# Kernel optimization log

Measured on AMD Instinct MI355X. Metric: run time of the kernel, lower is better.

The kernel has to match this reference:

```python
import jax, jax.numpy as jnp
import numpy as np

B, D = 200000, 128
K = 1024


def setup_inputs() -> dict:
    key = jax.random.key(0)
    k1, k2 = jax.random.split(key)
    x_BD = jax.random.normal(k1, (B, D), dtype=jnp.float32)
    codebook = jax.random.uniform(k2, (K, D), dtype=jnp.float32)
    return {"x_BD": x_BD, "codebook": codebook}


def reference(x_BD, codebook):
    x_sq_B1 = jnp.sum(x_BD * x_BD, axis=-1, keepdims=True)
    c_sq_K = jnp.sum(codebook * codebook, axis=-1)
    dists_BK = x_sq_B1 - 2.0 * jnp.einsum("bd,kd->bk", x_BD, codebook) + c_sq_K
    codes_B = jnp.argmin(dists_BK, axis=-1)  # [B] int
    quant_x_BD = codebook[codes_B]           # gather, [B, D]
    return quant_x_BD, codes_B
```

## Files before the change

### kernel.cpp

```cpp
#include <hip/hip_runtime.h>


typedef float v2f __attribute__((ext_vector_type(2)));

#define DDIM 128
#define KCODES 1024
#define BM 64
#define BN 256
#define DCH 16
#define NTILES (KCODES / BN)
#define NCHUNK (DDIM / DCH)

__global__ void csq_kernel(const float* __restrict__ cb, float* __restrict__ csq) {
    int k = blockIdx.x * blockDim.x + threadIdx.x;
    if (k >= KCODES) return;
    const float* __restrict__ c = cb + (long)k * DDIM;
    float s0 = 0.f, s1 = 0.f, s2 = 0.f, s3 = 0.f;
#pragma unroll
    for (int d = 0; d < DDIM; d += 4) {
        s0 = fmaf(c[d + 0], c[d + 0], s0);
        s1 = fmaf(c[d + 1], c[d + 1], s1);
        s2 = fmaf(c[d + 2], c[d + 2], s2);
        s3 = fmaf(c[d + 3], c[d + 3], s3);
    }
    csq[k] = (s0 + s1) + (s2 + s3);
}

#define PK_LO(a, xx, cc) \
    asm("v_pk_fma_f32 %0, %1, %2, %0 op_sel:[0,0,0] op_sel_hi:[0,1,1]" \
        : "+v"(a) : "v"(xx), "v"(cc))
#define PK_HI(a, xx, cc) \
    asm("v_pk_fma_f32 %0, %1, %2, %0 op_sel:[1,0,0] op_sel_hi:[1,1,1]" \
        : "+v"(a) : "v"(xx), "v"(cc))

__launch_bounds__(256, 3)
__global__ void vq_gemm_kernel(const float* __restrict__ x, const float* __restrict__ cb,
                               const float* __restrict__ csq, float* __restrict__ quant,
                               float* __restrict__ codes) {
    __shared__ float xs[DDIM * BM];
    __shared__ float cs[DCH * BN];
    __shared__ int win[BM];

    const int tid = threadIdx.x;
    const long r0 = (long)blockIdx.x * BM;

    {
        const int r = tid >> 2;
        const int qb = (tid & 3) * 8;
        const float* __restrict__ xrow = x + (r0 + r) * DDIM;
#pragma unroll
        for (int j = 0; j < 8; ++j) {
            const int q = qb + j;
            const float4 v = *(const float4*)(xrow + q * 4);
            xs[(q * 4 + 0) * BM + r] = v.x;
            xs[(q * 4 + 1) * BM + r] = v.y;
            xs[(q * 4 + 2) * BM + r] = v.z;
            xs[(q * 4 + 3) * BM + r] = v.w;
        }
    }
    __syncthreads();

    const int tr = tid >> 5;
    const int tc = tid & 31;

    float s[4][8];
#pragma unroll
    for (int a = 0; a < 4; ++a)
#pragma unroll
        for (int b = 0; b < 8; ++b) s[a][b] = 0.f;
#pragma unroll
    for (int d = 0; d < DDIM; d += 4) {
#pragma unroll
        for (int dd = 0; dd < 4; ++dd) {
            const float4 a0 = *(const float4*)&xs[(d + dd) * BM + tr * 8];
            const float4 a1 = *(const float4*)&xs[(d + dd) * BM + tr * 8 + 4];
            s[dd][0] = fmaf(a0.x, a0.x, s[dd][0]);
            s[dd][1] = fmaf(a0.y, a0.y, s[dd][1]);
            s[dd][2] = fmaf(a0.z, a0.z, s[dd][2]);
            s[dd][3] = fmaf(a0.w, a0.w, s[dd][3]);
            s[dd][4] = fmaf(a1.x, a1.x, s[dd][4]);
            s[dd][5] = fmaf(a1.y, a1.y, s[dd][5]);
            s[dd][6] = fmaf(a1.z, a1.z, s[dd][6]);
            s[dd][7] = fmaf(a1.w, a1.w, s[dd][7]);
        }
    }
    float xsq[8];
#pragma unroll
    for (int i = 0; i < 8; ++i) xsq[i] = (s[0][i] + s[1][i]) + (s[2][i] + s[3][i]);

    float best[8];
    int bidx[8];
#pragma unroll
    for (int i = 0; i < 8; ++i) { best[i] = 3.4e38f; bidx[i] = 0; }

#pragma unroll 1
    for (int ct = 0; ct < NTILES; ++ct) {
        v2f acc[8][4];
#pragma unroll
        for (int i = 0; i < 8; ++i)
#pragma unroll
            for (int jj = 0; jj < 4; ++jj) acc[i][jj] = (v2f){0.f, 0.f};

#pragma unroll 1
        for (int dc = 0; dc < NCHUNK; ++dc) {
            __syncthreads();
            {
                const float* __restrict__ crow =
                    cb + (long)(ct * BN + tid) * DDIM + dc * DCH;
#pragma unroll
                for (int j = 0; j < 4; ++j) {
                    const float4 v = *(const float4*)(crow + j * 4);
                    cs[(j * 4 + 0) * BN + tid] = v.x;
                    cs[(j * 4 + 1) * BN + tid] = v.y;
                    cs[(j * 4 + 2) * BN + tid] = v.z;
                    cs[(j * 4 + 3) * BN + tid] = v.w;
                }
            }
            __syncthreads();
#pragma unroll
            for (int d = 0; d < DCH; ++d) {
                const float4 xa0 = *(const float4*)&xs[(dc * DCH + d) * BM + tr * 8];
                const float4 xa1 = *(const float4*)&xs[(dc * DCH + d) * BM + tr * 8 + 4];
                const float4 ca0 = *(const float4*)&cs[d * BN + tc * 4];
                const float4 ca1 = *(const float4*)&cs[d * BN + 128 + tc * 4];
                v2f xp[4], cp[4];
                xp[0] = (v2f){xa0.x, xa0.y}; xp[1] = (v2f){xa0.z, xa0.w};
                xp[2] = (v2f){xa1.x, xa1.y}; xp[3] = (v2f){xa1.z, xa1.w};
                cp[0] = (v2f){ca0.x, ca0.y}; cp[1] = (v2f){ca0.z, ca0.w};
                cp[2] = (v2f){ca1.x, ca1.y}; cp[3] = (v2f){ca1.z, ca1.w};
#pragma unroll
                for (int jj = 0; jj < 4; ++jj) {
                    PK_LO(acc[0][jj], xp[0], cp[jj]);
                    PK_HI(acc[1][jj], xp[0], cp[jj]);
                    PK_LO(acc[2][jj], xp[1], cp[jj]);
                    PK_HI(acc[3][jj], xp[1], cp[jj]);
                    PK_LO(acc[4][jj], xp[2], cp[jj]);
                    PK_HI(acc[5][jj], xp[2], cp[jj]);
                    PK_LO(acc[6][jj], xp[3], cp[jj]);
                    PK_HI(acc[7][jj], xp[3], cp[jj]);
                }
            }
        }

        float csq_r[8];
#pragma unroll
        for (int j = 0; j < 4; ++j) {
            csq_r[j]     = csq[ct * BN + tc * 4 + j];
            csq_r[4 + j] = csq[ct * BN + 128 + tc * 4 + j];
        }
#pragma unroll
        for (int i = 0; i < 8; ++i) {
#pragma unroll
            for (int jj = 0; jj < 4; ++jj) {
#pragma unroll
                for (int h = 0; h < 2; ++h) {
                    const int jl = jj * 2 + h;
                    const int cj = ct * BN + ((jl < 4) ? (tc * 4 + jl) : (128 + tc * 4 + jl - 4));
                    const float dist = fmaf(-2.0f, acc[i][jj][h], xsq[i]) + csq_r[jl];
                    if (dist < best[i]) { best[i] = dist; bidx[i] = cj; }
                }
            }
        }
    }

#pragma unroll
    for (int i = 0; i < 8; ++i) {
#pragma unroll
        for (int off = 16; off >= 1; off >>= 1) {
            const float ov = __shfl_xor(best[i], off);
            const int ovi = __shfl_xor(bidx[i], off);
            if (ov < best[i] || (ov == best[i] && ovi < bidx[i])) {
                best[i] = ov; bidx[i] = ovi;
            }
        }
    }
    if (tc == 0) {
#pragma unroll
        for (int i = 0; i < 8; ++i) {
            const int r = tr * 8 + i;
            codes[r0 + r] = (float)bidx[i];
            win[r] = bidx[i];
        }
    }
    __syncthreads();

    {
        const int r = tid >> 2;
        const int qb = (tid & 3) * 8;
        const float* __restrict__ crow = cb + (long)win[r] * DDIM;
        float* __restrict__ qrow = quant + (r0 + r) * DDIM;
#pragma unroll
        for (int j = 0; j < 8; ++j) {
            const int q = qb + j;
            *(float4*)(qrow + q * 4) = *(const float4*)(crow + q * 4);
        }
    }
}

extern "C" void kernel_launch(void* const* d_in, const int* in_sizes, int n_in,
                              void* d_out, int out_size, void* d_ws, size_t ws_size,
                              hipStream_t stream) {
    const float* x  = (const float*)d_in[0];
    const float* cb = (const float*)d_in[1];
    const int B = in_sizes[0] / DDIM;

    float* quant = (float*)d_out;
    float* codes = (float*)d_out + (size_t)B * DDIM;
    float* csq   = (float*)d_ws;

    csq_kernel<<<(KCODES + 255) / 256, 256, 0, stream>>>(cb, csq);

    const int blocks = B / BM;
    vq_gemm_kernel<<<blocks, 256, 0, stream>>>(x, cb, csq, quant, codes);
}
```

Baseline: 791.2 us.

## Broadcast x rows via scalar loads, double-buffer codebook tiles in LDS

Each wavefront now owns 16 rows. The x values are fetched with s_load_dwordx2 into SGPRs and used as the scalar operand of v_pk_fma_f32, so the x tile is no longer staged in LDS. Codebook chunks are double-buffered in LDS with a register prefetch of the next chunk, which cuts the barriers per chunk from two to one. The row norms ||x||^2 are computed directly from global memory and broadcast with shuffles. The trade-offs are serialized scalar-load latency, since every sub-step waits on lgkmcnt(0), and more accumulator and register pressure.

```diff
diff --git a/kernel.cpp b/kernel.cpp
--- a/kernel.cpp
+++ b/kernel.cpp
@@ -2,6 +2,7 @@
 
 
 typedef float v2f __attribute__((ext_vector_type(2)));
+typedef int   v2i __attribute__((ext_vector_type(2)));
 
 #define DDIM 128
 #define KCODES 1024
@@ -26,161 +27,184 @@
     csq[k] = (s0 + s1) + (s2 + s3);
 }
 
-#define PK_LO(a, xx, cc) \
+#define PKL(a, xx, cc) \
     asm("v_pk_fma_f32 %0, %1, %2, %0 op_sel:[0,0,0] op_sel_hi:[0,1,1]" \
-        : "+v"(a) : "v"(xx), "v"(cc))
-#define PK_HI(a, xx, cc) \
+        : "+v"(a) : "s"(xx), "v"(cc))
+#define PKH(a, xx, cc) \
     asm("v_pk_fma_f32 %0, %1, %2, %0 op_sel:[1,0,0] op_sel_hi:[1,1,1]" \
-        : "+v"(a) : "v"(xx), "v"(cc))
+        : "+v"(a) : "s"(xx), "v"(cc))
+
+#define FOR16(M) M(0) M(1) M(2) M(3) M(4) M(5) M(6) M(7) \
+                 M(8) M(9) M(10) M(11) M(12) M(13) M(14) M(15)
 
 __launch_bounds__(256, 3)
 __global__ void vq_gemm_kernel(const float* __restrict__ x, const float* __restrict__ cb,
                                const float* __restrict__ csq, float* __restrict__ quant,
                                float* __restrict__ codes) {
-    __shared__ float xs[DDIM * BM];
-    __shared__ float cs[DCH * BN];
+    __shared__ float cs[2][DCH * BN];
     __shared__ int win[BM];
 
     const int tid = threadIdx.x;
     const long r0 = (long)blockIdx.x * BM;
+    const int lane = tid & 63;
+    const int wv = __builtin_amdgcn_readfirstlane(tid >> 6);
+    const int wr0 = wv * 16;
+
+    float xsq_mine = 0.f;
+    if (lane < 16) {
+        const float* __restrict__ xr = x + (r0 + wr0 + lane) * DDIM;
+        float s0 = 0.f, s1 = 0.f, s2 = 0.f, s3 = 0.f;
+#pragma unroll
+        for (int q = 0; q < 32; ++q) {
+            const float4 v = *(const float4*)(xr + q * 4);
+            s0 = fmaf(v.x, v.x, s0);
+            s1 = fmaf(v.y, v.y, s1);
+            s2 = fmaf(v.z, v.z, s2);
+            s3 = fmaf(v.w, v.w, s3);
+        }
+        xsq_mine = (s0 + s1) + (s2 + s3);
+    }
+    float xsqall[16];
+#pragma unroll
+    for (int r = 0; r < 16; ++r) xsqall[r] = __shfl(xsq_mine, r);
 
     {
-        const int r = tid >> 2;
-        const int qb = (tid & 3) * 8;
-        const float* __restrict__ xrow = x + (r0 + r) * DDIM;
-#pragma unroll
-        for (int j = 0; j < 8; ++j) {
-            const int q = qb + j;
-            const float4 v = *(const float4*)(xrow + q * 4);
-            xs[(q * 4 + 0) * BM + r] = v.x;
-            xs[(q * 4 + 1) * BM + r] = v.y;
-            xs[(q * 4 + 2) * BM + r] = v.z;
-            xs[(q * 4 + 3) * BM + r] = v.w;
+        const float* __restrict__ crow = cb + (long)tid * DDIM;
+#pragma unroll
+        for (int j = 0; j < 4; ++j) {
+            const float4 v = *(const float4*)(crow + j * 4);
+            cs[0][(j * 4 + 0) * BN + tid] = v.x;
+            cs[0][(j * 4 + 1) * BN + tid] = v.y;
+            cs[0][(j * 4 + 2) * BN + tid] = v.z;
+            cs[0][(j * 4 + 3) * BN + tid] = v.w;
         }
     }
     __syncthreads();
 
-    const int tr = tid >> 5;
-    const int tc = tid & 31;
-
-    float s[4][8];
-#pragma unroll
-    for (int a = 0; a < 4; ++a)
-#pragma unroll
-        for (int b = 0; b < 8; ++b) s[a][b] = 0.f;
-#pragma unroll
-    for (int d = 0; d < DDIM; d += 4) {
-#pragma unroll
-        for (int dd = 0; dd < 4; ++dd) {
-            const float4 a0 = *(const float4*)&xs[(d + dd) * BM + tr * 8];
-            const float4 a1 = *(const float4*)&xs[(d + dd) * BM + tr * 8 + 4];
-            s[dd][0] = fmaf(a0.x, a0.x, s[dd][0]);
-            s[dd][1] = fmaf(a0.y, a0.y, s[dd][1]);
-            s[dd][2] = fmaf(a0.z, a0.z, s[dd][2]);
-            s[dd][3] = fmaf(a0.w, a0.w, s[dd][3]);
-            s[dd][4] = fmaf(a1.x, a1.x, s[dd][4]);
-            s[dd][5] = fmaf(a1.y, a1.y, s[dd][5]);
-            s[dd][6] = fmaf(a1.z, a1.z, s[dd][6]);
-            s[dd][7] = fmaf(a1.w, a1.w, s[dd][7]);
-        }
-    }
-    float xsq[8];
-#pragma unroll
-    for (int i = 0; i < 8; ++i) xsq[i] = (s[0][i] + s[1][i]) + (s[2][i] + s[3][i]);
-
-    float best[8];
-    int bidx[8];
-#pragma unroll
-    for (int i = 0; i < 8; ++i) { best[i] = 3.4e38f; bidx[i] = 0; }
+    float best[16];
+    int bidx[16];
+#pragma unroll
+    for (int r = 0; r < 16; ++r) { best[r] = 3.4e38f; bidx[r] = 0; }
+
+    v2f acc[16][2];
 
 #pragma unroll 1
-    for (int ct = 0; ct < NTILES; ++ct) {
-        v2f acc[8][4];
-#pragma unroll
-        for (int i = 0; i < 8; ++i)
-#pragma unroll
-            for (int jj = 0; jj < 4; ++jj) acc[i][jj] = (v2f){0.f, 0.f};
-
+    for (int t = 0; t < NTILES * NCHUNK; ++t) {
+        const int ct = t >> 3;
+        const int dc = t & 7;
+        if (dc == 0) {
+#define ZA(R) acc[R][0] = (v2f){0.f, 0.f}; acc[R][1] = (v2f){0.f, 0.f};
+            FOR16(ZA)
+#undef ZA
+        }
+
+        float4 pf0, pf1, pf2, pf3;
+        if (t < NTILES * NCHUNK - 1) {
+            const int nt = t + 1;
+            const float* __restrict__ crow =
+                cb + (long)(((nt >> 3) * BN) + tid) * DDIM + (nt & 7) * DCH;
+            pf0 = *(const float4*)(crow + 0);
+            pf1 = *(const float4*)(crow + 4);
+            pf2 = *(const float4*)(crow + 8);
+            pf3 = *(const float4*)(crow + 12);
+        }
+
+        const float* csp = cs[t & 1];
 #pragma unroll 1
-        for (int dc = 0; dc < NCHUNK; ++dc) {
-            __syncthreads();
-            {
-                const float* __restrict__ crow =
-                    cb + (long)(ct * BN + tid) * DDIM + dc * DCH;
-#pragma unroll
-                for (int j = 0; j < 4; ++j) {
-                    const float4 v = *(const float4*)(crow + j * 4);
-                    cs[(j * 4 + 0) * BN + tid] = v.x;
-                    cs[(j * 4 + 1) * BN + tid] = v.y;
-                    cs[(j * 4 + 2) * BN + tid] = v.z;
-                    cs[(j * 4 + 3) * BN + tid] = v.w;
-                }
-            }
-            __syncthreads();
-#pragma unroll
-            for (int d = 0; d < DCH; ++d) {
-                const float4 xa0 = *(const float4*)&xs[(dc * DCH + d) * BM + tr * 8];
-                const float4 xa1 = *(const float4*)&xs[(dc * DCH + d) * BM + tr * 8 + 4];
-                const float4 ca0 = *(const float4*)&cs[d * BN + tc * 4];
-                const float4 ca1 = *(const float4*)&cs[d * BN + 128 + tc * 4];
-                v2f xp[4], cp[4];
-                xp[0] = (v2f){xa0.x, xa0.y}; xp[1] = (v2f){xa0.z, xa0.w};
-                xp[2] = (v2f){xa1.x, xa1.y}; xp[3] = (v2f){xa1.z, xa1.w};
-                cp[0] = (v2f){ca0.x, ca0.y}; cp[1] = (v2f){ca0.z, ca0.w};
-                cp[2] = (v2f){ca1.x, ca1.y}; cp[3] = (v2f){ca1.z, ca1.w};
-#pragma unroll
-                for (int jj = 0; jj < 4; ++jj) {
-                    PK_LO(acc[0][jj], xp[0], cp[jj]);
-                    PK_HI(acc[1][jj], xp[0], cp[jj]);
-                    PK_LO(acc[2][jj], xp[1], cp[jj]);
-                    PK_HI(acc[3][jj], xp[1], cp[jj]);
-                    PK_LO(acc[4][jj], xp[2], cp[jj]);
-                    PK_HI(acc[5][jj], xp[2], cp[jj]);
-                    PK_LO(acc[6][jj], xp[3], cp[jj]);
-                    PK_HI(acc[7][jj], xp[3], cp[jj]);
-                }
-            }
-        }
-
-        float csq_r[8];
-#pragma unroll
-        for (int j = 0; j < 4; ++j) {
-            csq_r[j]     = csq[ct * BN + tc * 4 + j];
-            csq_r[4 + j] = csq[ct * BN + 128 + tc * 4 + j];
-        }
-#pragma unroll
-        for (int i = 0; i < 8; ++i) {
-#pragma unroll
-            for (int jj = 0; jj < 4; ++jj) {
-#pragma unroll
-                for (int h = 0; h < 2; ++h) {
-                    const int jl = jj * 2 + h;
-                    const int cj = ct * BN + ((jl < 4) ? (tc * 4 + jl) : (128 + tc * 4 + jl - 4));
-                    const float dist = fmaf(-2.0f, acc[i][jj][h], xsq[i]) + csq_r[jl];
-                    if (dist < best[i]) { best[i] = dist; bidx[i] = cj; }
-                }
-            }
-        }
-    }
-
-#pragma unroll
-    for (int i = 0; i < 8; ++i) {
-#pragma unroll
-        for (int off = 16; off >= 1; off >>= 1) {
-            const float ov = __shfl_xor(best[i], off);
-            const int ovi = __shfl_xor(bidx[i], off);
-            if (ov < best[i] || (ov == best[i] && ovi < bidx[i])) {
-                best[i] = ov; bidx[i] = ovi;
-            }
-        }
-    }
-    if (tc == 0) {
-#pragma unroll
-        for (int i = 0; i < 8; ++i) {
-            const int r = tr * 8 + i;
-            codes[r0 + r] = (float)bidx[i];
-            win[r] = bidx[i];
-        }
+        for (int sub = 0; sub < 8; ++sub) {
+            const float* xb = x + (r0 + wr0) * DDIM + dc * DCH + sub * 2;
+            v2i xq0, xq1, xq2, xq3, xq4, xq5, xq6, xq7,
+                xq8, xq9, xq10, xq11, xq12, xq13, xq14, xq15;
+            asm volatile(
+                "s_load_dwordx2 %[a0],  %[xb], 0x0\n\t"
+                "s_load_dwordx2 %[a1],  %[xb], 0x200\n\t"
+                "s_load_dwordx2 %[a2],  %[xb], 0x400\n\t"
+                "s_load_dwordx2 %[a3],  %[xb], 0x600\n\t"
+                "s_load_dwordx2 %[a4],  %[xb], 0x800\n\t"
+                "s_load_dwordx2 %[a5],  %[xb], 0xa00\n\t"
+                "s_load_dwordx2 %[a6],  %[xb], 0xc00\n\t"
+                "s_load_dwordx2 %[a7],  %[xb], 0xe00\n\t"
+                "s_load_dwordx2 %[a8],  %[xb], 0x1000\n\t"
+                "s_load_dwordx2 %[a9],  %[xb], 0x1200\n\t"
+                "s_load_dwordx2 %[a10], %[xb], 0x1400\n\t"
+                "s_load_dwordx2 %[a11], %[xb], 0x1600\n\t"
+                "s_load_dwordx2 %[a12], %[xb], 0x1800\n\t"
+                "s_load_dwordx2 %[a13], %[xb], 0x1a00\n\t"
+                "s_load_dwordx2 %[a14], %[xb], 0x1c00\n\t"
+                "s_load_dwordx2 %[a15], %[xb], 0x1e00\n\t"
+                "s_waitcnt lgkmcnt(0)"
+                : [a0] "=s"(xq0), [a1] "=s"(xq1), [a2] "=s"(xq2), [a3] "=s"(xq3),
+                  [a4] "=s"(xq4), [a5] "=s"(xq5), [a6] "=s"(xq6), [a7] "=s"(xq7),
+                  [a8] "=s"(xq8), [a9] "=s"(xq9), [a10] "=s"(xq10), [a11] "=s"(xq11),
+                  [a12] "=s"(xq12), [a13] "=s"(xq13), [a14] "=s"(xq14), [a15] "=s"(xq15)
+                : [xb] "s"(xb));
+
+            const int dl = sub * 2;
+            const float4 ca  = *(const float4*)&csp[dl * BN + lane * 4];
+            const float4 cb4 = *(const float4*)&csp[(dl + 1) * BN + lane * 4];
+            v2f cp0 = (v2f){ca.x, ca.y},  cp1 = (v2f){ca.z, ca.w};
+            v2f cp2 = (v2f){cb4.x, cb4.y}, cp3 = (v2f){cb4.z, cb4.w};
+
+#define SL(R) PKL(acc[R][0], xq##R, cp0); PKL(acc[R][1], xq##R, cp1);
+            FOR16(SL)
+#undef SL
+#define SH(R) PKH(acc[R][0], xq##R, cp2); PKH(acc[R][1], xq##R, cp3);
+            FOR16(SH)
+#undef SH
+        }
+
+        if (t < NTILES * NCHUNK - 1) {
+            float* dst = cs[(t + 1) & 1];
+            dst[(0) * BN + tid]  = pf0.x;
+            dst[(1) * BN + tid]  = pf0.y;
+            dst[(2) * BN + tid]  = pf0.z;
+            dst[(3) * BN + tid]  = pf0.w;
+            dst[(4) * BN + tid]  = pf1.x;
+            dst[(5) * BN + tid]  = pf1.y;
+            dst[(6) * BN + tid]  = pf1.z;
+            dst[(7) * BN + tid]  = pf1.w;
+            dst[(8) * BN + tid]  = pf2.x;
+            dst[(9) * BN + tid]  = pf2.y;
+            dst[(10) * BN + tid] = pf2.z;
+            dst[(11) * BN + tid] = pf2.w;
+            dst[(12) * BN + tid] = pf3.x;
+            dst[(13) * BN + tid] = pf3.y;
+            dst[(14) * BN + tid] = pf3.z;
+            dst[(15) * BN + tid] = pf3.w;
+        }
+
+        if (dc == 7) {
+            const int cb0 = ct * BN + lane * 4;
+            const float4 cq = *(const float4*)&csq[cb0];
+#define EPI(R) { \
+            const float t0 = fmaf(-2.0f, acc[R][0][0], xsqall[R]) + cq.x; \
+            if (t0 < best[R]) { best[R] = t0; bidx[R] = cb0 + 0; } \
+            const float t1 = fmaf(-2.0f, acc[R][0][1], xsqall[R]) + cq.y; \
+            if (t1 < best[R]) { best[R] = t1; bidx[R] = cb0 + 1; } \
+            const float t2 = fmaf(-2.0f, acc[R][1][0], xsqall[R]) + cq.z; \
+            if (t2 < best[R]) { best[R] = t2; bidx[R] = cb0 + 2; } \
+            const float t3 = fmaf(-2.0f, acc[R][1][1], xsqall[R]) + cq.w; \
+            if (t3 < best[R]) { best[R] = t3; bidx[R] = cb0 + 3; } }
+            FOR16(EPI)
+#undef EPI
+        }
+        __syncthreads();
+    }
+
+#define RED(R) \
+    _Pragma("unroll") \
+    for (int off = 32; off >= 1; off >>= 1) { \
+        const float ov = __shfl_xor(best[R], off); \
+        const int oi = __shfl_xor(bidx[R], off); \
+        if (ov < best[R] || (ov == best[R] && oi < bidx[R])) { \
+            best[R] = ov; bidx[R] = oi; } }
+    FOR16(RED)
+#undef RED
+
+    if (lane == 0) {
+#define WRW(R) codes[r0 + wr0 + R] = (float)bidx[R]; win[wr0 + R] = bidx[R];
+        FOR16(WRW)
+#undef WRW
     }
     __syncthreads();
 
```

Result: slower. 831.7 us (+5.1%).
